# Performance work log

Hardware: AMD Instinct MI355X
Metric: run time of the kernel (lower is better)

Reference implementation:

```python
import jax, jax.numpy as jnp
import numpy as np

N = 50000   # number of cells/nodes
C = 256     # in_channels
H = 4       # num_heads
D = 64      # out_channels (per-head)
E = 800000  # number of edges (avg degree 16)


def setup_inputs() -> dict:
    key = jax.random.key(0)
    ks = jax.random.split(key, 10)
    s = 1.0 / np.sqrt(C)  # torch nn.Linear default init bound
    u = lambda k, shape: jax.random.uniform(k, shape, jnp.float32, -s, s)
    return {
        "query_input": jax.random.normal(ks[0], (N, C), jnp.float32),
        "source_input": jax.random.normal(ks[1], (N, C), jnp.float32),
        "Wq_w": u(ks[2], (H * D, C)), "Wq_b": u(ks[3], (H * D,)),
        "Wk_w": u(ks[4], (H * D, C)), "Wk_b": u(ks[5], (H * D,)),
        "Wv_w": u(ks[6], (H * D, C)), "Wv_b": u(ks[7], (H * D,)),
        "edge_index": jax.random.randint(ks[8], (2, E), 0, N),
        "edge_weight": jax.random.uniform(ks[9], (E,), jnp.float32),
    }


def reference(query_input, source_input, Wq_w, Wq_b, Wk_w, Wk_b, Wv_w, Wv_b,
              edge_index, edge_weight):
    n = query_input.shape[0]
    q = (query_input @ Wq_w.T + Wq_b).reshape(n, H, D)
    k = (source_input @ Wk_w.T + Wk_b).reshape(n, H, D)
    v = (source_input @ Wv_w.T + Wv_b).reshape(n, H, D)

    # --- linear (kernelized) attention, global Frobenius normalization ---
    qs = q / jnp.linalg.norm(q)
    ksn = k / jnp.linalg.norm(k)
    kvs = jnp.einsum('lhm,lhd->hmd', ksn, v)               # [H,M,D]
    attn_num = jnp.einsum('nhm,hmd->nhd', qs, kvs)
    attn_num = attn_num + v.sum(axis=0)[None]              # + vs_sum broadcast
    ks_sum = ksn.sum(axis=0)                               # [H,M]
    normalizer = jnp.einsum('nhm,hm->nh', qs, ks_sum)[..., None] + jnp.float32(n)
    attn_out = attn_num / normalizer                       # [N,H,D]

    # --- GCN aggregation on value: out[col] += w * d_norm_in * d_norm_out * v[row] ---
    row, col = edge_index[0], edge_index[1]
    d = jnp.zeros((n,), jnp.float32).at[col].add(1.0)      # in-degree on col
    d_norm_in = jnp.sqrt(1.0 / d[col])
    d_norm_out = jnp.sqrt(1.0 / d[row])
    val = jnp.nan_to_num(edge_weight * d_norm_in * d_norm_out,
                         nan=0.0, posinf=0.0, neginf=0.0)  # [E]
    gathered = v[row] * val[:, None, None]                 # [E,H,D]
    gcn_out = jax.ops.segment_sum(gathered, col, num_segments=n)  # [N,H,D]

    return (attn_out + gcn_out).mean(axis=1)               # [N,D]
```

## Files before the change

kernel.cpp:

```cpp
#include <hip/hip_runtime.h>
#include <hip/hip_bf16.h>

#define N_NODES 50000
#define N_EDGES 800000
#define NBUK 512
#define BWID 98
#define BCAP 2048
#define PCHUNK 2048
#define PBLK 391

typedef __bf16 bf16x8 __attribute__((ext_vector_type(8)));
typedef float f32x4 __attribute__((ext_vector_type(4)));

__device__ __forceinline__ unsigned short f2bf(float f) {
    unsigned int u = __builtin_bit_cast(unsigned int, f);
    u += 0x7fffu + ((u >> 16) & 1u);
    return (unsigned short)(u >> 16);
}

__global__ __launch_bounds__(256) void k_wprep(const float* __restrict__ Wv,
                                               const float* __restrict__ bv,
                                               unsigned short* __restrict__ wvbar,
                                               float* __restrict__ bvbar) {
    int idx = blockIdx.x * 256 + threadIdx.x;
    int d = idx >> 6;
    int c = (idx & 63) * 4;
    const float4* W4 = (const float4*)Wv;
    float4 w0 = W4[((d) * 256 + c) >> 2];
    float4 w1 = W4[((64 + d) * 256 + c) >> 2];
    float4 w2 = W4[((128 + d) * 256 + c) >> 2];
    float4 w3 = W4[((192 + d) * 256 + c) >> 2];
    ushort4 s;
    s.x = f2bf(0.25f * (w0.x + w1.x + w2.x + w3.x));
    s.y = f2bf(0.25f * (w0.y + w1.y + w2.y + w3.y));
    s.z = f2bf(0.25f * (w0.z + w1.z + w2.z + w3.z));
    s.w = f2bf(0.25f * (w0.w + w1.w + w2.w + w3.w));
    *(ushort4*)&wvbar[idx * 4] = s;
    if (blockIdx.x == 0 && threadIdx.x < 64) {
        int t = threadIdx.x;
        bvbar[t] = 0.25f * (bv[t] + bv[64 + t] + bv[128 + t] + bv[192 + t]);
    }
}

__global__ __launch_bounds__(256) void k_part(const int* __restrict__ ei,
                                              const float* __restrict__ ew,
                                              int* __restrict__ gcur,
                                              uint2* __restrict__ bkt)
{
    __shared__ int hist[NBUK];
    __shared__ int cur[NBUK];
    const int t = threadIdx.x;
    const int e0 = blockIdx.x * PCHUNK;
    hist[t] = 0; hist[t + 256] = 0;
    __syncthreads();
    #pragma unroll
    for (int k = 0; k < PCHUNK / 256; ++k) {
        int e = e0 + k * 256 + t;
        if (e < N_EDGES) {
            int c = ei[N_EDGES + e];
            atomicAdd(&hist[c / BWID], 1);
        }
    }
    __syncthreads();
    {
        int b = t;
        if (hist[b]) cur[b] = b * BCAP + atomicAdd(&gcur[b], hist[b]);
        b = t + 256;
        if (hist[b]) cur[b] = b * BCAP + atomicAdd(&gcur[b], hist[b]);
    }
    __syncthreads();
    #pragma unroll
    for (int k = 0; k < PCHUNK / 256; ++k) {
        int e = e0 + k * 256 + t;
        if (e < N_EDGES) {
            int c = ei[N_EDGES + e];
            int b = c / BWID;
            int row = ei[e];
            float w = ew[e];
            int slot = atomicAdd(&cur[b], 1);
            if (slot < (b + 1) * BCAP) {
                uint2 en;
                en.x = ((unsigned int)row << 16) | (unsigned int)f2bf(w);
                en.y = (unsigned int)(c - b * BWID);
                bkt[slot] = en;
            }
        }
    }
}

__global__ __launch_bounds__(256) void k_bucket(const int* __restrict__ gcur,
                                                const uint2* __restrict__ bkt,
                                                int* __restrict__ deg,
                                                int* __restrict__ off,
                                                unsigned int* __restrict__ srt)
{
    __shared__ int hist[128];
    __shared__ int lcur[128];
    const int t = threadIdx.x;
    const int b = blockIdx.x;
    if (t < 128) hist[t] = 0;
    __syncthreads();
    const int cnt = min(gcur[b], BCAP);
    const uint2* base = bkt + (size_t)b * BCAP;
    for (int i = t; i < cnt; i += 256)
        atomicAdd(&hist[base[i].y], 1);
    __syncthreads();
    const int v = (t < 128) ? hist[t] : 0;
    #pragma unroll
    for (int d = 1; d < 128; d <<= 1) {
        int u = (t >= d && t < 128) ? hist[t - d] : 0;
        __syncthreads();
        if (t >= d && t < 128) hist[t] += u;
        __syncthreads();
    }
    if (t < 128) {
        int excl = hist[t] - v;
        lcur[t] = excl;
        if (t < BWID) {
            int col = b * BWID + t;
            if (col < N_NODES) {
                deg[col] = v;
                off[col] = b * BCAP + excl;
            }
        }
    }
    __syncthreads();
    unsigned int* sb = srt + (size_t)b * BCAP;
    for (int i = t; i < cnt; i += 256) {
        uint2 en = base[i];
        int pos = atomicAdd(&lcur[en.y], 1);
        sb[pos] = en.x;
    }
}

__global__ __launch_bounds__(256, 2) void k_vbar(
    const float* __restrict__ Xs, const unsigned short* __restrict__ wvbar,
    const float* __restrict__ bvbar, const int* __restrict__ deg,
    float* __restrict__ vbar, float* __restrict__ vsumcol)
{
    __shared__ unsigned short lA[64 * 264];
    __shared__ unsigned short lB[64 * 264];
    __shared__ float lvs[64];
    const int t = threadIdx.x;
    const int n0 = blockIdx.x * 64;
    const int w = t >> 6;
    const int ln = t & 15;
    const int q = (t & 63) >> 4;

    if (t < 64) lvs[t] = 0.f;

    {
        const uint4* Wb = (const uint4*)wvbar;
        #pragma unroll
        for (int j = 0; j < 8; ++j) {
            int g = j * 256 + t;
            uint4 u = Wb[g];
            *(uint4*)&lB[(g >> 5) * 264 + (g & 31) * 8] = u;
        }
    }

    {
        const int r = t >> 2;
        const int cblk = (t & 3) * 16;
        const int g = n0 + r;
        const float4* X4 = (const float4*)Xs;
        if (g < N_NODES) {
            #pragma unroll
            for (int i = 0; i < 16; ++i) {
                float4 x = X4[g * 64 + cblk + i];
                ushort4 s;
                s.x = f2bf(x.x); s.y = f2bf(x.y); s.z = f2bf(x.z); s.w = f2bf(x.w);
                *(ushort4*)&lA[r * 264 + (cblk + i) * 4] = s;
            }
        } else {
            #pragma unroll
            for (int i = 0; i < 16; ++i)
                *(ushort4*)&lA[r * 264 + (cblk + i) * 4] = (ushort4){0, 0, 0, 0};
        }
    }
    __syncthreads();

    f32x4 acc[4];
    #pragma unroll
    for (int nf = 0; nf < 4; ++nf) acc[nf] = (f32x4){0.f, 0.f, 0.f, 0.f};

    #pragma unroll
    for (int ks = 0; ks < 8; ++ks) {
        bf16x8 a = *(const bf16x8*)&lA[(w * 16 + ln) * 264 + ks * 32 + q * 8];
        #pragma unroll
        for (int nf = 0; nf < 4; ++nf) {
            bf16x8 b = *(const bf16x8*)&lB[(nf * 16 + ln) * 264 + ks * 32 + q * 8];
            acc[nf] = __builtin_amdgcn_mfma_f32_16x16x32_bf16(a, b, acc[nf], 0, 0, 0);
        }
    }

    float bvb[4];
    #pragma unroll
    for (int nf = 0; nf < 4; ++nf) bvb[nf] = bvbar[nf * 16 + ln];
    float psum[4] = {0.f, 0.f, 0.f, 0.f};
    #pragma unroll
    for (int r4 = 0; r4 < 4; ++r4) {
        int g = n0 + w * 16 + q * 4 + r4;
        bool ok = g < N_NODES;
        float sc = 0.f;
        if (ok) {
            float dg = (float)deg[g];
            sc = (dg > 0.f) ? __frsqrt_rn(dg) : 0.f;
        }
        #pragma unroll
        for (int nf = 0; nf < 4; ++nf) {
            if (ok) vbar[g * 64 + nf * 16 + ln] = (acc[nf][r4] + bvb[nf]) * sc;
            psum[nf] += acc[nf][r4];
        }
    }
    #pragma unroll
    for (int nf = 0; nf < 4; ++nf) atomicAdd(&lvs[nf * 16 + ln], psum[nf]);
    __syncthreads();
    if (t < 64) atomicAdd(&vsumcol[t], lvs[t]);
}

__global__ __launch_bounds__(256) void k_gather(
    const int* __restrict__ off, const int* __restrict__ deg,
    const unsigned int* __restrict__ srt, const float* __restrict__ vbar,
    const float* __restrict__ vsumcol, const float* __restrict__ bvbar,
    float* __restrict__ out)
{
    const int t = threadIdx.x;
    const int lane = t & 63;
    const int n = blockIdx.x * 4 + (t >> 6);
    if (n >= N_NODES) return;
    const int e0 = off[n];
    const int dc = deg[n];
    const int e1 = e0 + dc;
    float acc = 0.f;
    int e = e0;
    for (; e + 3 < e1; e += 4) {
        unsigned int p0 = srt[e];
        unsigned int p1 = srt[e + 1];
        unsigned int p2 = srt[e + 2];
        unsigned int p3 = srt[e + 3];
        float a0 = __uint_as_float(p0 << 16) * vbar[(p0 >> 16) * 64 + lane];
        float a1 = __uint_as_float(p1 << 16) * vbar[(p1 >> 16) * 64 + lane];
        float a2 = __uint_as_float(p2 << 16) * vbar[(p2 >> 16) * 64 + lane];
        float a3 = __uint_as_float(p3 << 16) * vbar[(p3 >> 16) * 64 + lane];
        acc += (a0 + a1) + (a2 + a3);
    }
    for (; e < e1; ++e) {
        unsigned int p = srt[e];
        acc += __uint_as_float(p << 16) * vbar[(p >> 16) * 64 + lane];
    }
    float dcf = (float)dc;
    float scn = (dcf > 0.f) ? __frsqrt_rn(dcf) : 0.f;
    float aconst = vsumcol[lane] * (1.0f / (float)N_NODES) + bvbar[lane];
    out[n * 64 + lane] = acc * scn + aconst;
}

extern "C" void kernel_launch(void* const* d_in, const int* in_sizes, int n_in,
                              void* d_out, int out_size, void* d_ws, size_t ws_size,
                              hipStream_t stream)
{
    const float* Xs = (const float*)d_in[1];
    const float* Wv = (const float*)d_in[6];
    const float* bv = (const float*)d_in[7];
    const int*   ei = (const int*)d_in[8];
    const float* ew = (const float*)d_in[9];
    float* out = (float*)d_out;

    float* vbar = (float*)d_ws;
    uint2* bkt  = (uint2*)(vbar + (size_t)N_NODES * 64);
    unsigned int* srt = (unsigned int*)(bkt + (size_t)NBUK * BCAP);
    unsigned short* wvbar = (unsigned short*)(srt + (size_t)NBUK * BCAP);
    float* bvbar   = (float*)(wvbar + 16384);
    float* vsumcol = bvbar + 64;
    int*   gcur    = (int*)(vsumcol + 64);
    int*   deg     = gcur + NBUK;
    int*   off     = deg + N_NODES;

    hipMemsetAsync(vsumcol, 0, (size_t)(64 + NBUK) * 4, stream);
    k_wprep<<<16, 256, 0, stream>>>(Wv, bv, wvbar, bvbar);
    k_part<<<PBLK, 256, 0, stream>>>(ei, ew, gcur, bkt);
    k_bucket<<<NBUK, 256, 0, stream>>>(gcur, bkt, deg, off, srt);
    k_vbar<<<(N_NODES + 63) / 64, 256, 0, stream>>>(Xs, wvbar, bvbar, deg, vbar, vsumcol);
    k_gather<<<(NBUK * BWID) / 4, 256, 0, stream>>>(off, deg, srt, vbar, vsumcol, bvbar, out);
}
```

Before: 226.6 us.

## Store scaled value matrix in bf16 and read MFMA weights from pre-swizzled global layout

The per-node scaled value vector is now written as bf16 instead of fp32, which halves the bytes the random-access gather kernel fetches per edge and the bytes written by the projection kernel. The weight matrix is stored in MFMA fragment order so each lane loads its B operand directly from global memory (L2-resident). This removes the LDS weight tile, shrinks shared memory, and allows a higher occupancy launch bound. The cost is extra rounding error on the aggregated values.

After: 221.8 us. 2.1% less time.

```diff
diff --git a/kernel.cpp b/kernel.cpp
--- a/kernel.cpp
+++ b/kernel.cpp
@@ -17,6 +17,9 @@
     u += 0x7fffu + ((u >> 16) & 1u);
     return (unsigned short)(u >> 16);
 }
+__device__ __forceinline__ float bf2f(unsigned short s) {
+    return __uint_as_float((unsigned int)s << 16);
+}
 
 __global__ __launch_bounds__(256) void k_wprep(const float* __restrict__ Wv,
                                                const float* __restrict__ bv,
@@ -24,18 +27,24 @@
                                                float* __restrict__ bvbar) {
     int idx = blockIdx.x * 256 + threadIdx.x;
     int d = idx >> 6;
-    int c = (idx & 63) * 4;
+    int c0 = (idx & 63) * 4;
     const float4* W4 = (const float4*)Wv;
-    float4 w0 = W4[((d) * 256 + c) >> 2];
-    float4 w1 = W4[((64 + d) * 256 + c) >> 2];
-    float4 w2 = W4[((128 + d) * 256 + c) >> 2];
-    float4 w3 = W4[((192 + d) * 256 + c) >> 2];
+    float4 w0 = W4[((d) * 256 + c0) >> 2];
+    float4 w1 = W4[((64 + d) * 256 + c0) >> 2];
+    float4 w2 = W4[((128 + d) * 256 + c0) >> 2];
+    float4 w3 = W4[((192 + d) * 256 + c0) >> 2];
     ushort4 s;
     s.x = f2bf(0.25f * (w0.x + w1.x + w2.x + w3.x));
     s.y = f2bf(0.25f * (w0.y + w1.y + w2.y + w3.y));
     s.z = f2bf(0.25f * (w0.z + w1.z + w2.z + w3.z));
     s.w = f2bf(0.25f * (w0.w + w1.w + w2.w + w3.w));
-    *(ushort4*)&wvbar[idx * 4] = s;
+    int ks = c0 >> 5;
+    int q  = (c0 >> 3) & 3;
+    int j0 = c0 & 7;
+    int nf = d >> 4;
+    int ln = d & 15;
+    int base = ((ks * 4 + nf) * 64 + q * 16 + ln) * 8 + j0;
+    *(ushort4*)&wvbar[base] = s;
     if (blockIdx.x == 0 && threadIdx.x < 64) {
         int t = threadIdx.x;
         bvbar[t] = 0.25f * (bv[t] + bv[64 + t] + bv[128 + t] + bv[192 + t]);
@@ -133,31 +142,21 @@
     }
 }
 
-__global__ __launch_bounds__(256, 2) void k_vbar(
+__global__ __launch_bounds__(256, 4) void k_vbar(
     const float* __restrict__ Xs, const unsigned short* __restrict__ wvbar,
     const float* __restrict__ bvbar, const int* __restrict__ deg,
-    float* __restrict__ vbar, float* __restrict__ vsumcol)
+    unsigned short* __restrict__ vbarh, float* __restrict__ vsumcol)
 {
     __shared__ unsigned short lA[64 * 264];
-    __shared__ unsigned short lB[64 * 264];
     __shared__ float lvs[64];
     const int t = threadIdx.x;
     const int n0 = blockIdx.x * 64;
     const int w = t >> 6;
-    const int ln = t & 15;
-    const int q = (t & 63) >> 4;
+    const int l = t & 63;
+    const int ln = l & 15;
+    const int q = l >> 4;
 
     if (t < 64) lvs[t] = 0.f;
-
-    {
-        const uint4* Wb = (const uint4*)wvbar;
-        #pragma unroll
-        for (int j = 0; j < 8; ++j) {
-            int g = j * 256 + t;
-            uint4 u = Wb[g];
-            *(uint4*)&lB[(g >> 5) * 264 + (g & 31) * 8] = u;
-        }
-    }
 
     {
         const int r = t >> 2;
@@ -184,12 +183,13 @@
     #pragma unroll
     for (int nf = 0; nf < 4; ++nf) acc[nf] = (f32x4){0.f, 0.f, 0.f, 0.f};
 
+    const bf16x8* Wf = (const bf16x8*)wvbar;
     #pragma unroll
     for (int ks = 0; ks < 8; ++ks) {
         bf16x8 a = *(const bf16x8*)&lA[(w * 16 + ln) * 264 + ks * 32 + q * 8];
         #pragma unroll
         for (int nf = 0; nf < 4; ++nf) {
-            bf16x8 b = *(const bf16x8*)&lB[(nf * 16 + ln) * 264 + ks * 32 + q * 8];
+            bf16x8 b = Wf[(ks * 4 + nf) * 64 + l];
             acc[nf] = __builtin_amdgcn_mfma_f32_16x16x32_bf16(a, b, acc[nf], 0, 0, 0);
         }
     }
@@ -209,7 +209,7 @@
         }
         #pragma unroll
         for (int nf = 0; nf < 4; ++nf) {
-            if (ok) vbar[g * 64 + nf * 16 + ln] = (acc[nf][r4] + bvb[nf]) * sc;
+            if (ok) vbarh[g * 64 + nf * 16 + ln] = f2bf((acc[nf][r4] + bvb[nf]) * sc);
             psum[nf] += acc[nf][r4];
         }
     }
@@ -221,7 +221,7 @@
 
 __global__ __launch_bounds__(256) void k_gather(
     const int* __restrict__ off, const int* __restrict__ deg,
-    const unsigned int* __restrict__ srt, const float* __restrict__ vbar,
+    const unsigned int* __restrict__ srt, const unsigned short* __restrict__ vbarh,
     const float* __restrict__ vsumcol, const float* __restrict__ bvbar,
     float* __restrict__ out)
 {
@@ -239,15 +239,15 @@
         unsigned int p1 = srt[e + 1];
         unsigned int p2 = srt[e + 2];
         unsigned int p3 = srt[e + 3];
-        float a0 = __uint_as_float(p0 << 16) * vbar[(p0 >> 16) * 64 + lane];
-        float a1 = __uint_as_float(p1 << 16) * vbar[(p1 >> 16) * 64 + lane];
-        float a2 = __uint_as_float(p2 << 16) * vbar[(p2 >> 16) * 64 + lane];
-        float a3 = __uint_as_float(p3 << 16) * vbar[(p3 >> 16) * 64 + lane];
+        float a0 = __uint_as_float(p0 << 16) * bf2f(vbarh[(p0 >> 16) * 64 + lane]);
+        float a1 = __uint_as_float(p1 << 16) * bf2f(vbarh[(p1 >> 16) * 64 + lane]);
+        float a2 = __uint_as_float(p2 << 16) * bf2f(vbarh[(p2 >> 16) * 64 + lane]);
+        float a3 = __uint_as_float(p3 << 16) * bf2f(vbarh[(p3 >> 16) * 64 + lane]);
         acc += (a0 + a1) + (a2 + a3);
     }
     for (; e < e1; ++e) {
         unsigned int p = srt[e];
-        acc += __uint_as_float(p << 16) * vbar[(p >> 16) * 64 + lane];
+        acc += __uint_as_float(p << 16) * bf2f(vbarh[(p >> 16) * 64 + lane]);
     }
     float dcf = (float)dc;
     float scn = (dcf > 0.f) ? __frsqrt_rn(dcf) : 0.f;
@@ -266,8 +266,8 @@
     const float* ew = (const float*)d_in[9];
     float* out = (float*)d_out;
 
-    float* vbar = (float*)d_ws;
-    uint2* bkt  = (uint2*)(vbar + (size_t)N_NODES * 64);
+    unsigned short* vbarh = (unsigned short*)d_ws;
+    uint2* bkt  = (uint2*)(vbarh + (size_t)N_NODES * 64);
     unsigned int* srt = (unsigned int*)(bkt + (size_t)NBUK * BCAP);
     unsigned short* wvbar = (unsigned short*)(srt + (size_t)NBUK * BCAP);
     float* bvbar   = (float*)(wvbar + 16384);
@@ -280,6 +280,6 @@
     k_wprep<<<16, 256, 0, stream>>>(Wv, bv, wvbar, bvbar);
     k_part<<<PBLK, 256, 0, stream>>>(ei, ew, gcur, bkt);
     k_bucket<<<NBUK, 256, 0, stream>>>(gcur, bkt, deg, off, srt);
-    k_vbar<<<(N_NODES + 63) / 64, 256, 0, stream>>>(Xs, wvbar, bvbar, deg, vbar, vsumcol);
-    k_gather<<<(NBUK * BWID) / 4, 256, 0, stream>>>(off, deg, srt, vbar, vsumcol, bvbar, out);
-}
+    k_vbar<<<(N_NODES + 63) / 64, 256, 0, stream>>>(Xs, wvbar, bvbar, deg, vbarh, vsumcol);
+    k_gather<<<(NBUK * BWID) / 4, 256, 0, stream>>>(off, deg, srt, vbarh, vsumcol, bvbar, out);
+}
```
